# Kernel tuning notes

Hardware: AMD Instinct MI355X
Metric: run time of the kernel (lower is better)

The kernel has to match this reference:

```python
import jax, jax.numpy as jnp
import numpy as np

B, T, I, H, C = 64, 2048, 128, 256, 64


def setup_inputs() -> dict:
    key = jax.random.key(0)
    ks = jax.random.split(key, 12)
    s_ih = 1.0 / np.sqrt(H)
    inp = {
        "x": jax.random.normal(ks[0], (B, T, I), dtype=jnp.float32),
        # layer 0 GRU params (PyTorch layout: W_ih [3H, I], W_hh [3H, H])
        "W_ih0": jax.random.uniform(ks[1], (3 * H, I), minval=-s_ih, maxval=s_ih, dtype=jnp.float32),
        "W_hh0": jax.random.uniform(ks[2], (3 * H, H), minval=-s_ih, maxval=s_ih, dtype=jnp.float32),
        "b_ih0": jax.random.uniform(ks[3], (3 * H,), minval=-s_ih, maxval=s_ih, dtype=jnp.float32),
        "b_hh0": jax.random.uniform(ks[4], (3 * H,), minval=-s_ih, maxval=s_ih, dtype=jnp.float32),
        # layer 1 GRU params (input is H)
        "W_ih1": jax.random.uniform(ks[5], (3 * H, H), minval=-s_ih, maxval=s_ih, dtype=jnp.float32),
        "W_hh1": jax.random.uniform(ks[6], (3 * H, H), minval=-s_ih, maxval=s_ih, dtype=jnp.float32),
        "b_ih1": jax.random.uniform(ks[7], (3 * H,), minval=-s_ih, maxval=s_ih, dtype=jnp.float32),
        "b_hh1": jax.random.uniform(ks[8], (3 * H,), minval=-s_ih, maxval=s_ih, dtype=jnp.float32),
        # classifier head
        "fc_w": jax.random.uniform(ks[9], (C, H), minval=-s_ih, maxval=s_ih, dtype=jnp.float32),
        "fc_b": jax.random.uniform(ks[10], (C,), minval=-s_ih, maxval=s_ih, dtype=jnp.float32),
    }
    return inp


def _gru_layer(inp, W_ih, W_hh, b_ih, b_hh):
    # inp: [B, T, D_in] -> out: [B, T, H]; PyTorch GRU cell math.
    h_dim = W_hh.shape[1]
    # Precompute input-side gate pre-activations for the whole sequence (one big GEMM).
    gates_x = jnp.einsum("btd,gd->btg", inp, W_ih) + b_ih  # [B, T, 3H]

    def step(h, gx):
        gh = h @ W_hh.T + b_hh  # [B, 3H]
        xr, xz, xn = jnp.split(gx, 3, axis=-1)
        hr, hz, hn = jnp.split(gh, 3, axis=-1)
        r = jax.nn.sigmoid(xr + hr)
        z = jax.nn.sigmoid(xz + hz)
        n = jnp.tanh(xn + r * hn)
        h_new = (1.0 - z) * n + z * h
        return h_new, h_new

    h0 = jnp.zeros((inp.shape[0], h_dim), dtype=inp.dtype)
    _, out_tbh = jax.lax.scan(step, h0, jnp.swapaxes(gates_x, 0, 1))  # [T, B, H]
    return jnp.swapaxes(out_tbh, 0, 1)  # [B, T, H]


def reference(x, W_ih0, W_hh0, b_ih0, b_hh0, W_ih1, W_hh1, b_ih1, b_hh1, fc_w, fc_b):
    h = _gru_layer(x, W_ih0, W_hh0, b_ih0, b_hh0)
    h = _gru_layer(h, W_ih1, W_hh1, b_ih1, b_hh1)
    return h @ fc_w.T + fc_b  # [B, T, C]
```

## Files before the change

kernel.cpp:

```cpp
#include <hip/hip_runtime.h>

typedef _Float16 half2_t __attribute__((ext_vector_type(2)));
typedef _Float16 half8_t __attribute__((ext_vector_type(8)));
typedef float floatx4 __attribute__((ext_vector_type(4)));
typedef unsigned int u32;

#define BB 64
#define TT 2048
#define II 128
#define HH 256
#define CC 64
#define G3 (3*HH)
#define MTOT (BB*TT)

static __device__ __forceinline__ float dot2f(half2_t a, half2_t b, float c) {
#if __has_builtin(__builtin_amdgcn_fdot2)
    return __builtin_amdgcn_fdot2(a, b, c, false);
#else
    return c + (float)a[0]*(float)b[0] + (float)a[1]*(float)b[1];
#endif
}

static __device__ __forceinline__ half2_t bch2(u32 x) {
    return __builtin_bit_cast(half2_t, x);
}

static __device__ __forceinline__ float fast_rcp(float x) {
    return __builtin_amdgcn_rcpf(x);
}

static __device__ __forceinline__ float pair_sum(float x) {
    int i = __builtin_bit_cast(int, x);
    int a = __builtin_amdgcn_mov_dpp(i, 0xB1, 0xF, 0xF, true);
    return x + __builtin_bit_cast(float, a);
}
static __device__ __forceinline__ float dpp_xor2(float x) {
    int i = __builtin_bit_cast(int, x);
    int a = __builtin_amdgcn_mov_dpp(i, 0x4E, 0xF, 0xF, true);
    return __builtin_bit_cast(float, a);
}

template<typename AT, typename CT>
__global__ __launch_bounds__(256, 2)
void gemm_mfma(const AT* __restrict__ A, const float* __restrict__ W,
               const float* __restrict__ bias, CT* __restrict__ Cout,
               int M, int N, int K)
{
    __shared__ alignas(16) u32 As32[128 * 32];
    __shared__ alignas(16) u32 Bs32[64 * 32];

    const int tid  = threadIdx.x;
    const int lane = tid & 63;
    const int wave = tid >> 6;
    const int wm   = wave >> 1;
    const int wn   = wave & 1;
    const int m0   = blockIdx.y * 128;
    const int n0   = blockIdx.x * 64;
    const int lr   = lane & 15;
    const int lg   = lane >> 4;

    floatx4 acc[4][2] = {};

    for (int kc = 0; kc < K; kc += 64) {
        #pragma unroll
        for (int it = 0; it < 4; ++it) {
            const int s    = it * 256 + tid;
            const int row  = s >> 3;
            const int slot = s & 7;
            const AT* src  = A + (size_t)(m0 + row) * K + kc + slot * 8;
            half8_t v;
            if constexpr (sizeof(AT) == 2) {
                v = *reinterpret_cast<const half8_t*>(src);
            } else {
                const float4* s4 = reinterpret_cast<const float4*>(src);
                float4 lo = s4[0], hi = s4[1];
                v[0] = (_Float16)lo.x; v[1] = (_Float16)lo.y;
                v[2] = (_Float16)lo.z; v[3] = (_Float16)lo.w;
                v[4] = (_Float16)hi.x; v[5] = (_Float16)hi.y;
                v[6] = (_Float16)hi.z; v[7] = (_Float16)hi.w;
            }
            const int sw = slot ^ (row & 7);
            *reinterpret_cast<half8_t*>(&As32[row * 32 + sw * 4]) = v;
        }
        #pragma unroll
        for (int it = 0; it < 2; ++it) {
            const int s    = it * 256 + tid;
            const int row  = s >> 3;
            const int slot = s & 7;
            const float* src = W + (size_t)(n0 + row) * K + kc + slot * 8;
            const float4* s4 = reinterpret_cast<const float4*>(src);
            float4 lo = s4[0], hi = s4[1];
            half8_t v;
            v[0] = (_Float16)lo.x; v[1] = (_Float16)lo.y;
            v[2] = (_Float16)lo.z; v[3] = (_Float16)lo.w;
            v[4] = (_Float16)hi.x; v[5] = (_Float16)hi.y;
            v[6] = (_Float16)hi.z; v[7] = (_Float16)hi.w;
            const int sw = slot ^ (row & 7);
            *reinterpret_cast<half8_t*>(&Bs32[row * 32 + sw * 4]) = v;
        }
        __syncthreads();

        #pragma unroll
        for (int ks = 0; ks < 2; ++ks) {
            half8_t af[4], bf[2];
            #pragma unroll
            for (int fm = 0; fm < 4; ++fm) {
                const int row  = wm * 64 + fm * 16 + lr;
                const int slot = ks * 4 + lg;
                const int sw   = slot ^ (row & 7);
                af[fm] = *reinterpret_cast<const half8_t*>(&As32[row * 32 + sw * 4]);
            }
            #pragma unroll
            for (int fn = 0; fn < 2; ++fn) {
                const int row  = wn * 32 + fn * 16 + lr;
                const int slot = ks * 4 + lg;
                const int sw   = slot ^ (row & 7);
                bf[fn] = *reinterpret_cast<const half8_t*>(&Bs32[row * 32 + sw * 4]);
            }
            #pragma unroll
            for (int fm = 0; fm < 4; ++fm)
                #pragma unroll
                for (int fn = 0; fn < 2; ++fn)
                    acc[fm][fn] = __builtin_amdgcn_mfma_f32_16x16x32_f16(
                        af[fm], bf[fn], acc[fm][fn], 0, 0, 0);
        }
        __syncthreads();
    }

    #pragma unroll
    for (int fn = 0; fn < 2; ++fn) {
        const int n = n0 + wn * 32 + fn * 16 + lr;
        const float bv = bias[n];
        #pragma unroll
        for (int fm = 0; fm < 4; ++fm) {
            #pragma unroll
            for (int r = 0; r < 4; ++r) {
                const int m = m0 + wm * 64 + fm * 16 + lg * 4 + r;
                Cout[(size_t)m * N + n] = (CT)(acc[fm][fn][r] + bv);
            }
        }
    }
}

__global__ __attribute__((amdgpu_flat_work_group_size(512, 512),
                          amdgpu_waves_per_eu(2, 2)))
void gru_scan(const _Float16* __restrict__ gx,
              const float* __restrict__ Whh,
              const float* __restrict__ bhh,
              _Float16* __restrict__ hout)
{
    const int b  = blockIdx.x;
    const int t  = threadIdx.x;
    const int j  = t >> 1;
    const int kh = t & 1;

    half2_t w0[64], w1[64], w2[64];
    {
        const float2* q0 = reinterpret_cast<const float2*>(Whh + (size_t)j * HH + kh * 128);
        const float2* q1 = q0 + 128 * HH;
        const float2* q2 = q0 + 256 * HH;
        #pragma unroll
        for (int i = 0; i < 64; ++i) {
            const float2 a = q0[i], c = q1[i], d = q2[i];
            w0[i] = half2_t{(_Float16)a.x, (_Float16)a.y};
            w1[i] = half2_t{(_Float16)c.x, (_Float16)c.y};
            w2[i] = half2_t{(_Float16)d.x, (_Float16)d.y};
        }
    }
    const float bh_r = bhh[j], bh_z = bhh[HH + j], bh_n = bhh[2*HH + j];

    __shared__ alignas(16) u32 HsU[2][136];
    if (t < 272) reinterpret_cast<u32*>(HsU)[t] = 0u;
    float hprev = 0.f;

    const _Float16* gp = gx + (size_t)b * TT * G3 + j;
    u32* opw = (u32*)(hout + (size_t)b * TT * HH);

    _Float16 pxr = gp[0], pxz = gp[HH], pxn = gp[2*HH];
    __syncthreads();

    for (int step = 0; step < TT; ++step) {
        const _Float16 nxr = gp[G3];
        const _Float16 nxz = gp[G3 + HH];
        const _Float16 nxn = gp[G3 + 2*HH];

        const uint4* hb = reinterpret_cast<const uint4*>(HsU[step & 1] + kh * 68);
        float ar = 0.f, az = 0.f, an = 0.f;
        #pragma unroll
        for (int c = 0; c < 16; ++c) {
            const uint4 hv = hb[c];
            const half2_t ha = bch2(hv.x), hc = bch2(hv.y);
            const half2_t hd = bch2(hv.z), he = bch2(hv.w);
            ar = dot2f(ha, w0[4*c+0], ar); az = dot2f(ha, w1[4*c+0], az); an = dot2f(ha, w2[4*c+0], an);
            ar = dot2f(hc, w0[4*c+1], ar); az = dot2f(hc, w1[4*c+1], az); an = dot2f(hc, w2[4*c+1], an);
            ar = dot2f(hd, w0[4*c+2], ar); az = dot2f(hd, w1[4*c+2], az); an = dot2f(hd, w2[4*c+2], an);
            ar = dot2f(he, w0[4*c+3], ar); az = dot2f(he, w1[4*c+3], az); an = dot2f(he, w2[4*c+3], an);
        }
        ar = pair_sum(ar);
        az = pair_sum(az);
        an = pair_sum(an);

        const float r = fast_rcp(1.f + __expf(-((float)pxr + ar + bh_r)));
        const float z = fast_rcp(1.f + __expf(-((float)pxz + az + bh_z)));
        const float e = __expf(2.f * ((float)pxn + r * (an + bh_n)));
        const float n = 1.f - 2.f * fast_rcp(e + 1.f);
        const float hnew = (1.f - z) * n + z * hprev;
        hprev = hnew;

        const float hoth = dpp_xor2(hnew);
        if ((t & 3) == 0) {
            const half2_t hp{(_Float16)hnew, (_Float16)hoth};
            const u32 pu = __builtin_bit_cast(u32, hp);
            const int m = t >> 2;
            HsU[(step + 1) & 1][(m >> 6) * 68 + (m & 63)] = pu;
            opw[m] = pu;
        }
        asm volatile("s_waitcnt lgkmcnt(0)" ::: "memory");
        __builtin_amdgcn_s_barrier();

        gp += G3; opw += HH/2;
        pxr = nxr; pxz = nxz; pxn = nxn;
    }
}

extern "C" void kernel_launch(void* const* d_in, const int* in_sizes, int n_in,
                              void* d_out, int out_size, void* d_ws, size_t ws_size,
                              hipStream_t stream) {
    const float* x    = (const float*)d_in[0];
    const float* Wih0 = (const float*)d_in[1];
    const float* Whh0 = (const float*)d_in[2];
    const float* bih0 = (const float*)d_in[3];
    const float* bhh0 = (const float*)d_in[4];
    const float* Wih1 = (const float*)d_in[5];
    const float* Whh1 = (const float*)d_in[6];
    const float* bih1 = (const float*)d_in[7];
    const float* bhh1 = (const float*)d_in[8];
    const float* fcw  = (const float*)d_in[9];
    const float* fcb  = (const float*)d_in[10];
    float* out = (float*)d_out;

    _Float16* gxbuf = (_Float16*)d_ws;
    _Float16* hbuf  = (_Float16*)((char*)d_ws + (size_t)MTOT * G3 * sizeof(_Float16));

    const dim3 blk(256);
    gemm_mfma<float, _Float16><<<dim3(G3/64, MTOT/128), blk, 0, stream>>>(
        x, Wih0, bih0, gxbuf, MTOT, G3, II);
    gru_scan<<<dim3(BB), dim3(512), 0, stream>>>(gxbuf, Whh0, bhh0, hbuf);
    gemm_mfma<_Float16, _Float16><<<dim3(G3/64, MTOT/128), blk, 0, stream>>>(
        hbuf, Wih1, bih1, gxbuf, MTOT, G3, HH);
    gru_scan<<<dim3(BB), dim3(512), 0, stream>>>(gxbuf, Whh1, bhh1, hbuf);
    gemm_mfma<_Float16, float><<<dim3(CC/64, MTOT/128), blk, 0, stream>>>(
        hbuf, fcw, fcb, out, MTOT, CC, HH);
}
```

Measured before the change: 4.672 ms.

## Fuse layer-0 scan, layer-1 input GEMM and layer-1 scan into one flag-pipelined kernel

Replaces the separate layer-0 scan, layer-1 input GEMM and layer-1 scan launches with one persistent kernel. Block roles are assigned by block index. The layer-0 scan publishes per-batch progress every 16 steps. GEMM tiles wait until their 128-step chunk is ready, then compute it and bump a done counter, which the layer-1 scan polls before consuming each chunk. The aim is to overlap the two sequential recurrences instead of running them back to back. The cost is spin-waiting blocks that occupy CU slots, reliance on low-index blocks being scheduled first (otherwise it can deadlock), and use of the output buffer as scratch for the flags.

New measurement: 9.692 ms. +107.4%, slower.

```diff
diff --git a/kernel.cpp b/kernel.cpp
--- a/kernel.cpp
+++ b/kernel.cpp
@@ -142,14 +142,12 @@
     }
 }
 
-__global__ __attribute__((amdgpu_flat_work_group_size(512, 512),
-                          amdgpu_waves_per_eu(2, 2)))
-void gru_scan(const _Float16* __restrict__ gx,
-              const float* __restrict__ Whh,
-              const float* __restrict__ bhh,
-              _Float16* __restrict__ hout)
+template<int LAYER>
+static __device__ __forceinline__
+void scan_core(int b, const _Float16* __restrict__ gx,
+               const float* __restrict__ Whh, const float* __restrict__ bhh,
+               _Float16* __restrict__ hout, u32* prog, u32* done, u32* HsU)
 {
-    const int b  = blockIdx.x;
     const int t  = threadIdx.x;
     const int j  = t >> 1;
     const int kh = t & 1;
@@ -169,22 +167,41 @@
     }
     const float bh_r = bhh[j], bh_z = bhh[HH + j], bh_n = bhh[2*HH + j];
 
-    __shared__ alignas(16) u32 HsU[2][136];
-    if (t < 272) reinterpret_cast<u32*>(HsU)[t] = 0u;
+    if (t < 272) HsU[t] = 0u;
     float hprev = 0.f;
 
     const _Float16* gp = gx + (size_t)b * TT * G3 + j;
     u32* opw = (u32*)(hout + (size_t)b * TT * HH);
 
+    if (LAYER == 1) {
+        if (t == 0)
+            while (__hip_atomic_load(&done[b * 16], __ATOMIC_ACQUIRE,
+                                     __HIP_MEMORY_SCOPE_AGENT) < 12u)
+                __builtin_amdgcn_s_sleep(16);
+        __builtin_amdgcn_s_barrier();
+        __threadfence();
+    }
+
     _Float16 pxr = gp[0], pxz = gp[HH], pxn = gp[2*HH];
     __syncthreads();
 
     for (int step = 0; step < TT; ++step) {
+        if (LAYER == 1) {
+            const int nx = step + 1;
+            if ((nx & 127) == 0 && nx < TT) {
+                if (t == 0)
+                    while (__hip_atomic_load(&done[b * 16 + (nx >> 7)], __ATOMIC_ACQUIRE,
+                                             __HIP_MEMORY_SCOPE_AGENT) < 12u)
+                        __builtin_amdgcn_s_sleep(16);
+                __builtin_amdgcn_s_barrier();
+                __threadfence();
+            }
+        }
         const _Float16 nxr = gp[G3];
         const _Float16 nxz = gp[G3 + HH];
         const _Float16 nxn = gp[G3 + 2*HH];
 
-        const uint4* hb = reinterpret_cast<const uint4*>(HsU[step & 1] + kh * 68);
+        const uint4* hb = reinterpret_cast<const uint4*>(HsU + (step & 1) * 136 + kh * 68);
         float ar = 0.f, az = 0.f, an = 0.f;
         #pragma unroll
         for (int c = 0; c < 16; ++c) {
@@ -212,14 +229,148 @@
             const half2_t hp{(_Float16)hnew, (_Float16)hoth};
             const u32 pu = __builtin_bit_cast(u32, hp);
             const int m = t >> 2;
-            HsU[(step + 1) & 1][(m >> 6) * 68 + (m & 63)] = pu;
+            HsU[((step + 1) & 1) * 136 + (m >> 6) * 68 + (m & 63)] = pu;
             opw[m] = pu;
         }
         asm volatile("s_waitcnt lgkmcnt(0)" ::: "memory");
         __builtin_amdgcn_s_barrier();
 
+        if (LAYER == 0 && (step & 15) == 15) {
+            __threadfence();
+            __builtin_amdgcn_s_barrier();
+            if (t == 0)
+                __hip_atomic_store(&prog[b], (u32)(step + 1), __ATOMIC_RELEASE,
+                                   __HIP_MEMORY_SCOPE_AGENT);
+        }
+
         gp += G3; opw += HH/2;
         pxr = nxr; pxz = nxz; pxn = nxn;
+    }
+}
+
+static __device__ void gemm_role(int gid, const _Float16* __restrict__ hsrc,
+                                 const float* __restrict__ W, const float* __restrict__ bias,
+                                 _Float16* __restrict__ gout, u32* prog, u32* done, u32* SH)
+{
+    const int nt = gid % 12;
+    const int y  = gid / 12;
+    const int tc = y >> 6;
+    const int bb = y & 63;
+    const int tid = threadIdx.x;
+
+    if (tid == 0) {
+        const u32 need = (u32)((tc + 1) * 128);
+        while (__hip_atomic_load(&prog[bb], __ATOMIC_ACQUIRE,
+                                 __HIP_MEMORY_SCOPE_AGENT) < need)
+            __builtin_amdgcn_s_sleep(32);
+    }
+    __syncthreads();
+    __threadfence();
+
+    u32* As32 = SH;
+    u32* Bs32 = SH + 128 * 32;
+
+    const int lane = tid & 63;
+    const int wave = tid >> 6;
+    const int wm   = wave >> 1;
+    const int wn   = wave & 1;
+    const size_t m0 = (size_t)bb * TT + (size_t)tc * 128;
+    const int n0   = nt * 64;
+    const int lr   = lane & 15;
+    const int lg   = lane >> 4;
+
+    floatx4 acc[2][2] = {};
+
+    for (int kc = 0; kc < HH; kc += 64) {
+        #pragma unroll
+        for (int it = 0; it < 2; ++it) {
+            const int s    = it * 512 + tid;
+            const int row  = s >> 3;
+            const int slot = s & 7;
+            const _Float16* src = hsrc + (m0 + row) * HH + kc + slot * 8;
+            const half8_t v = *reinterpret_cast<const half8_t*>(src);
+            const int sw = slot ^ (row & 7);
+            *reinterpret_cast<half8_t*>(&As32[row * 32 + sw * 4]) = v;
+        }
+        {
+            const int row  = tid >> 3;
+            const int slot = tid & 7;
+            const float* src = W + (size_t)(n0 + row) * HH + kc + slot * 8;
+            const float4 lo = reinterpret_cast<const float4*>(src)[0];
+            const float4 hi = reinterpret_cast<const float4*>(src)[1];
+            half8_t v;
+            v[0] = (_Float16)lo.x; v[1] = (_Float16)lo.y;
+            v[2] = (_Float16)lo.z; v[3] = (_Float16)lo.w;
+            v[4] = (_Float16)hi.x; v[5] = (_Float16)hi.y;
+            v[6] = (_Float16)hi.z; v[7] = (_Float16)hi.w;
+            const int sw = slot ^ (row & 7);
+            *reinterpret_cast<half8_t*>(&Bs32[row * 32 + sw * 4]) = v;
+        }
+        __syncthreads();
+
+        #pragma unroll
+        for (int ks = 0; ks < 2; ++ks) {
+            half8_t af[2], bf[2];
+            #pragma unroll
+            for (int fm = 0; fm < 2; ++fm) {
+                const int row  = wm * 32 + fm * 16 + lr;
+                const int slot = ks * 4 + lg;
+                const int sw   = slot ^ (row & 7);
+                af[fm] = *reinterpret_cast<const half8_t*>(&As32[row * 32 + sw * 4]);
+            }
+            #pragma unroll
+            for (int fn = 0; fn < 2; ++fn) {
+                const int row  = wn * 32 + fn * 16 + lr;
+                const int slot = ks * 4 + lg;
+                const int sw   = slot ^ (row & 7);
+                bf[fn] = *reinterpret_cast<const half8_t*>(&Bs32[row * 32 + sw * 4]);
+            }
+            #pragma unroll
+            for (int fm = 0; fm < 2; ++fm)
+                #pragma unroll
+                for (int fn = 0; fn < 2; ++fn)
+                    acc[fm][fn] = __builtin_amdgcn_mfma_f32_16x16x32_f16(
+                        af[fm], bf[fn], acc[fm][fn], 0, 0, 0);
+        }
+        __syncthreads();
+    }
+
+    #pragma unroll
+    for (int fn = 0; fn < 2; ++fn) {
+        const int n = n0 + wn * 32 + fn * 16 + lr;
+        const float bv = bias[n];
+        #pragma unroll
+        for (int fm = 0; fm < 2; ++fm) {
+            #pragma unroll
+            for (int r = 0; r < 4; ++r) {
+                const size_t m = m0 + wm * 32 + fm * 16 + lg * 4 + r;
+                gout[m * G3 + n] = (_Float16)(acc[fm][fn][r] + bv);
+            }
+        }
+    }
+    __threadfence();
+    __syncthreads();
+    if (tid == 0) atomicAdd(&done[bb * 16 + tc], 1u);
+}
+
+__global__ __attribute__((amdgpu_flat_work_group_size(512, 512),
+                          amdgpu_waves_per_eu(2, 2)))
+void fused_mid(_Float16* __restrict__ gxbuf, _Float16* __restrict__ hbuf,
+               const float* __restrict__ Whh0, const float* __restrict__ bhh0,
+               const float* __restrict__ Wih1, const float* __restrict__ bih1,
+               const float* __restrict__ Whh1, const float* __restrict__ bhh1,
+               u32* flags)
+{
+    __shared__ alignas(16) u32 SH[6144];
+    u32* prog = flags;
+    u32* done = flags + 64;
+    const int bid = blockIdx.x;
+    if (bid < BB) {
+        scan_core<0>(bid, gxbuf, Whh0, bhh0, hbuf, prog, done, SH);
+    } else if (bid < 2 * BB) {
+        scan_core<1>(bid - BB, gxbuf, Whh1, bhh1, hbuf, prog, done, SH);
+    } else {
+        gemm_role(bid - 2 * BB, hbuf, Wih1, bih1, gxbuf, prog, done, SH);
     }
 }
 
@@ -242,13 +393,13 @@
     _Float16* gxbuf = (_Float16*)d_ws;
     _Float16* hbuf  = (_Float16*)((char*)d_ws + (size_t)MTOT * G3 * sizeof(_Float16));
 
-    const dim3 blk(256);
-    gemm_mfma<float, _Float16><<<dim3(G3/64, MTOT/128), blk, 0, stream>>>(
+    u32* flags = (u32*)d_out;
+    hipMemsetAsync(d_out, 0, (64 + 64 * 16) * sizeof(u32), stream);
+
+    gemm_mfma<float, _Float16><<<dim3(G3/64, MTOT/128), dim3(256), 0, stream>>>(
         x, Wih0, bih0, gxbuf, MTOT, G3, II);
-    gru_scan<<<dim3(BB), dim3(512), 0, stream>>>(gxbuf, Whh0, bhh0, hbuf);
-    gemm_mfma<_Float16, _Float16><<<dim3(G3/64, MTOT/128), blk, 0, stream>>>(
-        hbuf, Wih1, bih1, gxbuf, MTOT, G3, HH);
-    gru_scan<<<dim3(BB), dim3(512), 0, stream>>>(gxbuf, Whh1, bhh1, hbuf);
-    gemm_mfma<_Float16, float><<<dim3(CC/64, MTOT/128), blk, 0, stream>>>(
+    fused_mid<<<dim3(2 * BB + 12 * 1024), dim3(512), 0, stream>>>(
+        gxbuf, hbuf, Whh0, bhh0, Wih1, bih1, Whh1, bhh1, flags);
+    gemm_mfma<_Float16, float><<<dim3(CC/64, MTOT/128), dim3(256), 0, stream>>>(
         hbuf, fcw, fcb, out, MTOT, CC, HH);
 }
```
